# Performance work log

Hardware: AMD Instinct MI355X
Metric: run time of the kernel (lower is better)

## Reference

```python
import jax, jax.numpy as jnp
import numpy as np

N, FIN, FOUT = 4096, 512, 256
ALPHA = 0.2          # LeakyReLU negative slope
NEG_INF = -9e15      # mask value from the torch source


def setup_inputs() -> dict:
    key = jax.random.key(0)
    ks = jax.random.split(key, 11)
    h = jax.random.normal(ks[0], (N, FIN), dtype=jnp.float32)
    adj_n = jax.random.randint(ks[1], (N, N), 0, 2, dtype=jnp.int32)
    adj_d = jax.random.randint(ks[2], (N, N), 0, 2, dtype=jnp.int32)
    G_nd = jax.random.normal(ks[3], (2, N, FOUT), dtype=jnp.float32)
    # learned parameters (xavier-ish scale)
    W_n = jax.random.normal(ks[4], (FIN, FOUT), dtype=jnp.float32) * 0.05
    a1_n = jax.random.normal(ks[5], (FOUT, 1), dtype=jnp.float32) * 0.05
    a2_n = jax.random.normal(ks[6], (FOUT, 1), dtype=jnp.float32) * 0.05
    W_d = jax.random.normal(ks[7], (FIN, FOUT), dtype=jnp.float32) * 0.05
    a1_d = jax.random.normal(ks[8], (FOUT, 1), dtype=jnp.float32) * 0.05
    a2_d = jax.random.normal(ks[9], (FOUT, 1), dtype=jnp.float32) * 0.05
    scale = jnp.zeros((1,), dtype=jnp.float32)
    return {"h": h, "adj_n": adj_n, "adj_d": adj_d, "G_nd": G_nd,
            "W_n": W_n, "a1_n": a1_n, "a2_n": a2_n,
            "W_d": W_d, "a1_d": a1_d, "a2_d": a2_d, "scale": scale}


def _gat(h, adj, W, a1, a2):
    # Wh: [N, FOUT]
    Wh = h @ W
    # outer-sum attention logits: e[i,j] = leakyrelu(Wh_i.a1 + Wh_j.a2)
    e = jax.nn.leaky_relu((Wh @ a1) + (Wh @ a2).T, negative_slope=ALPHA)  # [N, N]
    att = jnp.where(adj > 0, e, jnp.float32(NEG_INF))
    att = jax.nn.softmax(att, axis=-1)
    # dropout is identity in eval mode
    return jax.nn.elu(att @ Wh)  # [N, FOUT]


def reference(h, adj_n, adj_d, G_nd, W_n, a1_n, a2_n, W_d, a1_d, a2_d, scale):
    f_n_S = _gat(h, adj_n, W_n, a1_n, a2_n)
    f_d_S = _gat(h, adj_d, W_d, a1_d, a2_d)
    # The G_nd cross-attention branch (f_nd_C) in the torch source is computed
    # but never used in the returned value; omitted here (jit would DCE it).
    return f_n_S + f_d_S
```

## Files before the change

### kernel.cpp

```cpp
#include <hip/hip_runtime.h>

#define N_NODES 4096
#define FIN     512
#define FOUT    256
#define NSPLIT  4
#define NTILES  ((N_NODES / NSPLIT) / 64)
#define ITILE   128

typedef __attribute__((ext_vector_type(8))) short bf16x8s;
typedef __attribute__((ext_vector_type(4))) float f32x4;
typedef __attribute__((ext_vector_type(8))) unsigned short u16x8;
typedef unsigned short u16;
typedef unsigned int   u32;

__device__ inline u16 f2b(float f) {
    union { float f; unsigned int u; } v; v.f = f;
    unsigned int r = v.u + 0x7fffu + ((v.u >> 16) & 1u);
    return (u16)(r >> 16);
}

__global__ __launch_bounds__(256) void prep_kernel(
    const float* __restrict__ h, const float* __restrict__ Wn,
    const float* __restrict__ Wd,
    u16* __restrict__ hb, u16* __restrict__ WTb, float* __restrict__ s12)
{
    __shared__ u16 tl[64 * 72];
    const int t = threadIdx.x;
    const int bid = blockIdx.x;

    if (bid < 1024) {
        int idx = (bid * 256 + t) * 8;
        float4 f0 = *(const float4*)&h[idx];
        float4 f1 = *(const float4*)&h[idx + 4];
        u16x8 o;
        o[0]=f2b(f0.x); o[1]=f2b(f0.y); o[2]=f2b(f0.z); o[3]=f2b(f0.w);
        o[4]=f2b(f1.x); o[5]=f2b(f1.y); o[6]=f2b(f1.z); o[7]=f2b(f1.w);
        *(u16x8*)&hb[idx] = o;
    } else if (bid < 1088) {
        int id = bid - 1024;
        int kx = id & 7, ny = (id >> 3) & 3, b = id >> 5;
        const float* W = b ? Wd : Wn;
        int k0 = kx * 64, n0 = ny * 64;
        int kr = t >> 2, nc0 = (t & 3) * 16;
        const float* src = W + (size_t)(k0 + kr) * FOUT + n0 + nc0;
        #pragma unroll
        for (int jv = 0; jv < 4; ++jv) {
            float4 f = *(const float4*)(src + jv * 4);
            tl[(nc0 + jv * 4 + 0) * 72 + kr] = f2b(f.x);
            tl[(nc0 + jv * 4 + 1) * 72 + kr] = f2b(f.y);
            tl[(nc0 + jv * 4 + 2) * 72 + kr] = f2b(f.z);
            tl[(nc0 + jv * 4 + 3) * 72 + kr] = f2b(f.w);
        }
        __syncthreads();
        int n = t >> 2, kc0 = (t & 3) * 16;
        u16* dst = WTb + ((size_t)b << 17) + (size_t)(n0 + n) * FIN + k0 + kc0;
        *(uint4*)dst       = *(uint4*)&tl[n * 72 + kc0];
        *(uint4*)(dst + 8) = *(uint4*)&tl[n * 72 + kc0 + 8];
    } else {
        float4 z = {0.f, 0.f, 0.f, 0.f};
        float4* p4 = (float4*)s12;
        #pragma unroll
        for (int k = 0; k < 16; ++k) p4[k * 256 + t] = z;
    }
}

__global__ __launch_bounds__(256) void wh_gemm_kernel(
    const u16* __restrict__ hb, const u16* __restrict__ WTb,
    const float* __restrict__ a1n, const float* __restrict__ a2n,
    const float* __restrict__ a1d, const float* __restrict__ a2d,
    u16* __restrict__ WhT, float* __restrict__ s1, float* __restrict__ s2)
{
    __shared__ u16 smem[8192];
    u16* a_lds = smem;
    u16* b_lds = smem + 4096;

    const int t = threadIdx.x, lane = t & 63, w = t >> 6;
    const int q = lane >> 4, ln = lane & 15;
    const int i0 = blockIdx.x * 64, n0 = blockIdx.y * 64, b = blockIdx.z;
    const u16* wt = WTb + ((size_t)b << 17);

    f32x4 acc[4];
    #pragma unroll
    for (int i = 0; i < 4; ++i) acc[i] = (f32x4){0.f, 0.f, 0.f, 0.f};

    for (int kt = 0; kt < 8; ++kt) {
        const int k0 = kt * 64;
        __syncthreads();
        #pragma unroll
        for (int it = 0; it < 2; ++it) {
            int chunk = it * 256 + t;
            int r = chunk >> 3, kc = chunk & 7;
            const u16* g = hb + (size_t)(i0 + r) * FIN + k0 + ((kc ^ (r & 7)) * 8);
            u16* l = a_lds + (it * 256 + w * 64) * 8;
            __builtin_amdgcn_global_load_lds(
                (const __attribute__((address_space(1))) void*)g,
                (__attribute__((address_space(3))) void*)l, 16, 0, 0);
        }
        #pragma unroll
        for (int it = 0; it < 2; ++it) {
            int chunk = it * 256 + t;
            int n = chunk >> 3, kc = chunk & 7;
            const u16* g = wt + (size_t)(n0 + n) * FIN + k0 + ((kc ^ (n & 7)) * 8);
            u16* l = b_lds + (it * 256 + w * 64) * 8;
            __builtin_amdgcn_global_load_lds(
                (const __attribute__((address_space(1))) void*)g,
                (__attribute__((address_space(3))) void*)l, 16, 0, 0);
        }
        __syncthreads();
        #pragma unroll
        for (int ks = 0; ks < 2; ++ks) {
            int sw = ((ks * 4 + q) ^ (ln & 7)) * 8;
            bf16x8s af = *(const bf16x8s*)&a_lds[(w * 16 + ln) * 64 + sw];
            #pragma unroll
            for (int nt = 0; nt < 4; ++nt) {
                bf16x8s bfv = *(const bf16x8s*)&b_lds[(nt * 16 + ln) * 64 + sw];
                acc[nt] = __builtin_amdgcn_mfma_f32_16x16x32_bf16(af, bfv, acc[nt], 0, 0, 0);
            }
        }
    }

    {
        const float* a1 = b ? a1d : a1n;
        const float* a2 = b ? a2d : a2n;
        float s1p[4] = {0.f, 0.f, 0.f, 0.f};
        float s2p[4] = {0.f, 0.f, 0.f, 0.f};
        #pragma unroll
        for (int nt = 0; nt < 4; ++nt) {
            float va1 = a1[n0 + nt * 16 + ln];
            float va2 = a2[n0 + nt * 16 + ln];
            #pragma unroll
            for (int r = 0; r < 4; ++r) {
                s1p[r] += acc[nt][r] * va1;
                s2p[r] += acc[nt][r] * va2;
            }
        }
        #pragma unroll
        for (int r = 0; r < 4; ++r) {
            #pragma unroll
            for (int off = 8; off >= 1; off >>= 1) {
                s1p[r] += __shfl_xor(s1p[r], off);
                s2p[r] += __shfl_xor(s2p[r], off);
            }
            if (ln == 0) {
                int row = i0 + w * 16 + q * 4 + r;
                atomicAdd(&s1[b * N_NODES + row], s1p[r]);
                atomicAdd(&s2[b * N_NODES + row], s2p[r]);
            }
        }
    }

    __syncthreads();
    #pragma unroll
    for (int nt = 0; nt < 4; ++nt)
        #pragma unroll
        for (int r = 0; r < 4; ++r)
            smem[(nt * 16 + ln) * 72 + (w * 16 + q * 4 + r)] = f2b(acc[nt][r]);
    __syncthreads();
    {
        const int nl = t >> 2, is = (t & 3) * 16;
        u16* dst = WhT + ((size_t)b << 20) + (size_t)(n0 + nl) * N_NODES + i0 + is;
        *(uint4*)dst       = *(uint4*)&smem[nl * 72 + is];
        *(uint4*)(dst + 8) = *(uint4*)&smem[nl * 72 + is + 8];
    }
}

__global__ __launch_bounds__(1024) void attn_kernel(
    const int* __restrict__ adj_n, const int* __restrict__ adj_d,
    const u16* __restrict__ WhT,
    const float* __restrict__ s1, const float* __restrict__ s2,
    float* __restrict__ num_ws, float* __restrict__ den_ws)
{
    __shared__ u16 wht_lds[256 * 64];
    __shared__ u16 p_lds[128 * 64];

    const int t = threadIdx.x, lane = t & 63, w = t >> 6;
    const int q = lane >> 4, ln = lane & 15;
    const int ih = w >> 2;
    const int nq = w & 3;
    const int b = blockIdx.z, split = blockIdx.y;
    const int i0 = blockIdx.x * ITILE;

    const int* adjb = b ? adj_d : adj_n;
    const u16* whtB = WhT + ((size_t)b << 20);
    const float* s1b = s1 + b * N_NODES;
    const float* s2b = s2 + b * N_NODES;

    const int pr = t >> 3;
    const int cw = t & 7;
    const int pc = cw * 8;
    const float s1v = s1b[i0 + pr];
    const size_t arow = (size_t)(i0 + pr) * N_NODES + pc;
    const int swp = (cw ^ (pr & 7)) * 8;

    float den0 = 0.f;

    f32x4 acc[2][4];
    #pragma unroll
    for (int mt = 0; mt < 2; ++mt)
        #pragma unroll
        for (int nt = 0; nt < 4; ++nt) acc[mt][nt] = (f32x4){0.f, 0.f, 0.f, 0.f};

    const int jbase = split * (N_NODES / NSPLIT);

    int4 a0_pf = *(const int4*)&adjb[arow + jbase];
    int4 a1_pf = *(const int4*)&adjb[arow + jbase + 4];
    float4 sv0_pf = *(const float4*)&s2b[jbase + pc];
    float4 sv1_pf = *(const float4*)&s2b[jbase + pc + 4];

    for (int jt = 0; jt < NTILES; ++jt) {
        const int j0 = jbase + jt * 64;
        __syncthreads();
        #pragma unroll
        for (int it = 0; it < 2; ++it) {
            int chunk = it * 1024 + t;
            int n = chunk >> 3, kc = chunk & 7;
            const u16* g = whtB + (size_t)n * N_NODES + j0 + ((kc ^ (n & 7)) * 8);
            u16* l = wht_lds + (it * 1024 + w * 64) * 8;
            __builtin_amdgcn_global_load_lds(
                (const __attribute__((address_space(1))) void*)g,
                (__attribute__((address_space(3))) void*)l, 16, 0, 0);
        }
        int4 a0 = a0_pf, a1 = a1_pf;
        float4 sv0 = sv0_pf, sv1 = sv1_pf;
        if (jt < NTILES - 1) {
            const int jn = j0 + 64;
            a0_pf = *(const int4*)&adjb[arow + jn];
            a1_pf = *(const int4*)&adjb[arow + jn + 4];
            sv0_pf = *(const float4*)&s2b[jn + pc];
            sv1_pf = *(const float4*)&s2b[jn + pc + 4];
        }
        int v[8] = {a0.x, a0.y, a0.z, a0.w, a1.x, a1.y, a1.z, a1.w};
        float svf[8] = {sv0.x, sv0.y, sv0.z, sv0.w, sv1.x, sv1.y, sv1.z, sv1.w};
        float d = 0.f;
        u16x8 pk;
        #pragma unroll
        for (int jj = 0; jj < 8; ++jj) {
            float x = s1v + svf[jj];
            float p = (v[jj] > 0) ? __expf(fmaxf(x, 0.2f * x)) : 0.f;
            d += p;
            pk[jj] = f2b(p);
        }
        d += __shfl_down(d, 4, 8);
        d += __shfl_down(d, 2, 8);
        d += __shfl_down(d, 1, 8);
        if ((t & 7) == 0) den0 += d;
        *(u16x8*)&p_lds[pr * 64 + swp] = pk;
        __syncthreads();
        #pragma unroll
        for (int ks = 0; ks < 2; ++ks) {
            int sw = ((ks * 4 + q) ^ (ln & 7)) * 8;
            bf16x8s af0 = *(const bf16x8s*)&p_lds[(ih * 32 + 0 * 16 + ln) * 64 + sw];
            bf16x8s af1 = *(const bf16x8s*)&p_lds[(ih * 32 + 1 * 16 + ln) * 64 + sw];
            #pragma unroll
            for (int nt = 0; nt < 4; ++nt) {
                bf16x8s bfv = *(const bf16x8s*)&wht_lds[(nq * 64 + nt * 16 + ln) * 64 + sw];
                acc[0][nt] = __builtin_amdgcn_mfma_f32_16x16x32_bf16(af0, bfv, acc[0][nt], 0, 0, 0);
                acc[1][nt] = __builtin_amdgcn_mfma_f32_16x16x32_bf16(af1, bfv, acc[1][nt], 0, 0, 0);
            }
        }
    }
    const size_t pbase = (size_t)(b * NSPLIT + split) * N_NODES;
    #pragma unroll
    for (int mt = 0; mt < 2; ++mt)
        #pragma unroll
        for (int r = 0; r < 4; ++r) {
            int row = ih * 32 + mt * 16 + q * 4 + r;
            #pragma unroll
            for (int nt = 0; nt < 4; ++nt)
                num_ws[(pbase + i0 + row) * FOUT + nq * 64 + nt * 16 + ln] = acc[mt][nt][r];
        }
    if ((t & 7) == 0) den_ws[pbase + i0 + pr] = den0;
}

__global__ __launch_bounds__(256) void reduce_kernel(
    const float* __restrict__ num_ws, const float* __restrict__ den_ws,
    float* __restrict__ out)
{
    int gid = blockIdx.x * 256 + threadIdx.x;
    int i = gid >> 6;
    int f4 = (gid & 63) * 4;
    float4 o = {0.f, 0.f, 0.f, 0.f};
    #pragma unroll
    for (int b = 0; b < 2; ++b) {
        float4 num = {0.f, 0.f, 0.f, 0.f};
        float den = 0.f;
        #pragma unroll
        for (int s = 0; s < NSPLIT; ++s) {
            const float4 v = *(const float4*)&num_ws[((size_t)(b * NSPLIT + s) * N_NODES + i) * FOUT + f4];
            num.x += v.x; num.y += v.y; num.z += v.z; num.w += v.w;
            den += den_ws[(size_t)(b * NSPLIT + s) * N_NODES + i];
        }
        float inv = 1.0f / den;
        float e0 = num.x * inv, e1 = num.y * inv, e2 = num.z * inv, e3 = num.w * inv;
        o.x += (e0 > 0.f) ? e0 : expm1f(e0);
        o.y += (e1 > 0.f) ? e1 : expm1f(e1);
        o.z += (e2 > 0.f) ? e2 : expm1f(e2);
        o.w += (e3 > 0.f) ? e3 : expm1f(e3);
    }
    *(float4*)&out[(size_t)i * FOUT + f4] = o;
}

extern "C" void kernel_launch(void* const* d_in, const int* in_sizes, int n_in,
                              void* d_out, int out_size, void* d_ws, size_t ws_size,
                              hipStream_t stream) {
    const float* h    = (const float*)d_in[0];
    const int*   adjn = (const int*)d_in[1];
    const int*   adjd = (const int*)d_in[2];
    const float* Wn   = (const float*)d_in[4];
    const float* a1n  = (const float*)d_in[5];
    const float* a2n  = (const float*)d_in[6];
    const float* Wd   = (const float*)d_in[7];
    const float* a1d  = (const float*)d_in[8];
    const float* a2d  = (const float*)d_in[9];

    char* ws = (char*)d_ws;
    u16*  WhT  = (u16*)ws;
    float* s1  = (float*)(ws + ((size_t)8 << 20));
    float* s2  = s1 + 2 * N_NODES;
    float* den = s2 + 2 * N_NODES;
    u16*  hb   = (u16*)(ws + ((size_t)8 << 20) + ((size_t)256 << 10));
    u16*  WTb  = (u16*)(ws + ((size_t)12 << 20) + ((size_t)256 << 10));
    float* num = (float*)(ws + ((size_t)8 << 20) + ((size_t)256 << 10));

    prep_kernel<<<1089, 256, 0, stream>>>(h, Wn, Wd, hb, WTb, s1);
    wh_gemm_kernel<<<dim3(64, 4, 2), 256, 0, stream>>>(hb, WTb, a1n, a2n, a1d, a2d, WhT, s1, s2);
    attn_kernel<<<dim3(N_NODES / ITILE, NSPLIT, 2), 1024, 0, stream>>>(adjn, adjd, WhT, s1, s2, num, den);
    reduce_kernel<<<1024, 256, 0, stream>>>(num, den, (float*)d_out);
}
```

Before: 215.9 us.

## Load MFMA B operands directly from global memory and double-buffer P tile

Both the Wh GEMM and the attention kernel stop staging operand tiles in LDS through global_load_lds and instead read each wave's MFMA fragments straight from global memory. The attention kernel keeps P in LDS but double-buffers it, which removes one barrier per tile. This cuts LDS traffic and synchronisation. In exchange, each WhT fragment is now re-read from global/L2 by the waves sharing it (every ih wave group) instead of being shared through LDS, and uncoalesced 16-byte row-strided loads with exposed latency may hurt.

After: 247.1 us. 14.5% more time.

```diff
diff --git a/kernel.cpp b/kernel.cpp
--- a/kernel.cpp
+++ b/kernel.cpp
@@ -70,52 +70,37 @@
     const float* __restrict__ a1d, const float* __restrict__ a2d,
     u16* __restrict__ WhT, float* __restrict__ s1, float* __restrict__ s2)
 {
-    __shared__ u16 smem[8192];
-    u16* a_lds = smem;
-    u16* b_lds = smem + 4096;
+    __shared__ u16 smem[64 * 72];
 
     const int t = threadIdx.x, lane = t & 63, w = t >> 6;
     const int q = lane >> 4, ln = lane & 15;
     const int i0 = blockIdx.x * 64, n0 = blockIdx.y * 64, b = blockIdx.z;
     const u16* wt = WTb + ((size_t)b << 17);
 
+    const u16* arow = hb + (size_t)(i0 + w * 16 + ln) * FIN;
+    const u16* brow0 = wt + (size_t)(n0 + 0 * 16 + ln) * FIN;
+    const u16* brow1 = wt + (size_t)(n0 + 1 * 16 + ln) * FIN;
+    const u16* brow2 = wt + (size_t)(n0 + 2 * 16 + ln) * FIN;
+    const u16* brow3 = wt + (size_t)(n0 + 3 * 16 + ln) * FIN;
+
     f32x4 acc[4];
     #pragma unroll
     for (int i = 0; i < 4; ++i) acc[i] = (f32x4){0.f, 0.f, 0.f, 0.f};
 
+    #pragma unroll
     for (int kt = 0; kt < 8; ++kt) {
-        const int k0 = kt * 64;
-        __syncthreads();
-        #pragma unroll
-        for (int it = 0; it < 2; ++it) {
-            int chunk = it * 256 + t;
-            int r = chunk >> 3, kc = chunk & 7;
-            const u16* g = hb + (size_t)(i0 + r) * FIN + k0 + ((kc ^ (r & 7)) * 8);
-            u16* l = a_lds + (it * 256 + w * 64) * 8;
-            __builtin_amdgcn_global_load_lds(
-                (const __attribute__((address_space(1))) void*)g,
-                (__attribute__((address_space(3))) void*)l, 16, 0, 0);
-        }
-        #pragma unroll
-        for (int it = 0; it < 2; ++it) {
-            int chunk = it * 256 + t;
-            int n = chunk >> 3, kc = chunk & 7;
-            const u16* g = wt + (size_t)(n0 + n) * FIN + k0 + ((kc ^ (n & 7)) * 8);
-            u16* l = b_lds + (it * 256 + w * 64) * 8;
-            __builtin_amdgcn_global_load_lds(
-                (const __attribute__((address_space(1))) void*)g,
-                (__attribute__((address_space(3))) void*)l, 16, 0, 0);
-        }
-        __syncthreads();
         #pragma unroll
         for (int ks = 0; ks < 2; ++ks) {
-            int sw = ((ks * 4 + q) ^ (ln & 7)) * 8;
-            bf16x8s af = *(const bf16x8s*)&a_lds[(w * 16 + ln) * 64 + sw];
-            #pragma unroll
-            for (int nt = 0; nt < 4; ++nt) {
-                bf16x8s bfv = *(const bf16x8s*)&b_lds[(nt * 16 + ln) * 64 + sw];
-                acc[nt] = __builtin_amdgcn_mfma_f32_16x16x32_bf16(af, bfv, acc[nt], 0, 0, 0);
-            }
+            const int ko = kt * 64 + (ks * 4 + q) * 8;
+            bf16x8s af = *(const bf16x8s*)&arow[ko];
+            bf16x8s b0 = *(const bf16x8s*)&brow0[ko];
+            bf16x8s b1 = *(const bf16x8s*)&brow1[ko];
+            bf16x8s b2 = *(const bf16x8s*)&brow2[ko];
+            bf16x8s b3 = *(const bf16x8s*)&brow3[ko];
+            acc[0] = __builtin_amdgcn_mfma_f32_16x16x32_bf16(af, b0, acc[0], 0, 0, 0);
+            acc[1] = __builtin_amdgcn_mfma_f32_16x16x32_bf16(af, b1, acc[1], 0, 0, 0);
+            acc[2] = __builtin_amdgcn_mfma_f32_16x16x32_bf16(af, b2, acc[2], 0, 0, 0);
+            acc[3] = __builtin_amdgcn_mfma_f32_16x16x32_bf16(af, b3, acc[3], 0, 0, 0);
         }
     }
 
@@ -170,8 +155,7 @@
     const float* __restrict__ s1, const float* __restrict__ s2,
     float* __restrict__ num_ws, float* __restrict__ den_ws)
 {
-    __shared__ u16 wht_lds[256 * 64];
-    __shared__ u16 p_lds[128 * 64];
+    __shared__ u16 p_lds[2][128 * 64];
 
     const int t = threadIdx.x, lane = t & 63, w = t >> 6;
     const int q = lane >> 4, ln = lane & 15;
@@ -185,6 +169,11 @@
     const float* s1b = s1 + b * N_NODES;
     const float* s2b = s2 + b * N_NODES;
 
+    const u16* brow0 = whtB + (size_t)(nq * 64 + 0 * 16 + ln) * N_NODES;
+    const u16* brow1 = whtB + (size_t)(nq * 64 + 1 * 16 + ln) * N_NODES;
+    const u16* brow2 = whtB + (size_t)(nq * 64 + 2 * 16 + ln) * N_NODES;
+    const u16* brow3 = whtB + (size_t)(nq * 64 + 3 * 16 + ln) * N_NODES;
+
     const int pr = t >> 3;
     const int cw = t & 7;
     const int pc = cw * 8;
@@ -209,17 +198,8 @@
 
     for (int jt = 0; jt < NTILES; ++jt) {
         const int j0 = jbase + jt * 64;
-        __syncthreads();
-        #pragma unroll
-        for (int it = 0; it < 2; ++it) {
-            int chunk = it * 1024 + t;
-            int n = chunk >> 3, kc = chunk & 7;
-            const u16* g = whtB + (size_t)n * N_NODES + j0 + ((kc ^ (n & 7)) * 8);
-            u16* l = wht_lds + (it * 1024 + w * 64) * 8;
-            __builtin_amdgcn_global_load_lds(
-                (const __attribute__((address_space(1))) void*)g,
-                (__attribute__((address_space(3))) void*)l, 16, 0, 0);
-        }
+        const int cur = jt & 1;
+
         int4 a0 = a0_pf, a1 = a1_pf;
         float4 sv0 = sv0_pf, sv1 = sv1_pf;
         if (jt < NTILES - 1) {
@@ -244,19 +224,26 @@
         d += __shfl_down(d, 2, 8);
         d += __shfl_down(d, 1, 8);
         if ((t & 7) == 0) den0 += d;
-        *(u16x8*)&p_lds[pr * 64 + swp] = pk;
+        *(u16x8*)&p_lds[cur][pr * 64 + swp] = pk;
         __syncthreads();
         #pragma unroll
         for (int ks = 0; ks < 2; ++ks) {
-            int sw = ((ks * 4 + q) ^ (ln & 7)) * 8;
-            bf16x8s af0 = *(const bf16x8s*)&p_lds[(ih * 32 + 0 * 16 + ln) * 64 + sw];
-            bf16x8s af1 = *(const bf16x8s*)&p_lds[(ih * 32 + 1 * 16 + ln) * 64 + sw];
-            #pragma unroll
-            for (int nt = 0; nt < 4; ++nt) {
-                bf16x8s bfv = *(const bf16x8s*)&wht_lds[(nq * 64 + nt * 16 + ln) * 64 + sw];
-                acc[0][nt] = __builtin_amdgcn_mfma_f32_16x16x32_bf16(af0, bfv, acc[0][nt], 0, 0, 0);
-                acc[1][nt] = __builtin_amdgcn_mfma_f32_16x16x32_bf16(af1, bfv, acc[1][nt], 0, 0, 0);
-            }
+            const int sw = ((ks * 4 + q) ^ (ln & 7)) * 8;
+            const int ko = j0 + (ks * 4 + q) * 8;
+            bf16x8s af0 = *(const bf16x8s*)&p_lds[cur][(ih * 32 + 0 * 16 + ln) * 64 + sw];
+            bf16x8s af1 = *(const bf16x8s*)&p_lds[cur][(ih * 32 + 1 * 16 + ln) * 64 + sw];
+            bf16x8s b0 = *(const bf16x8s*)&brow0[ko];
+            bf16x8s b1 = *(const bf16x8s*)&brow1[ko];
+            bf16x8s b2 = *(const bf16x8s*)&brow2[ko];
+            bf16x8s b3 = *(const bf16x8s*)&brow3[ko];
+            acc[0][0] = __builtin_amdgcn_mfma_f32_16x16x32_bf16(af0, b0, acc[0][0], 0, 0, 0);
+            acc[1][0] = __builtin_amdgcn_mfma_f32_16x16x32_bf16(af1, b0, acc[1][0], 0, 0, 0);
+            acc[0][1] = __builtin_amdgcn_mfma_f32_16x16x32_bf16(af0, b1, acc[0][1], 0, 0, 0);
+            acc[1][1] = __builtin_amdgcn_mfma_f32_16x16x32_bf16(af1, b1, acc[1][1], 0, 0, 0);
+            acc[0][2] = __builtin_amdgcn_mfma_f32_16x16x32_bf16(af0, b2, acc[0][2], 0, 0, 0);
+            acc[1][2] = __builtin_amdgcn_mfma_f32_16x16x32_bf16(af1, b2, acc[1][2], 0, 0, 0);
+            acc[0][3] = __builtin_amdgcn_mfma_f32_16x16x32_bf16(af0, b3, acc[0][3], 0, 0, 0);
+            acc[1][3] = __builtin_amdgcn_mfma_f32_16x16x32_bf16(af1, b3, acc[1][3], 0, 0, 0);
         }
     }
     const size_t pbase = (size_t)(b * NSPLIT + split) * N_NODES;
```

## Fuse prep, GEMM, attention and reduce into one cooperative kernel

Applied to the files above, without the earlier changes.

Merges the four launches (bf16 conversion/transpose, Wh GEMM with score projections, masked-softmax attention GEMM, split reduction with ELU) into one cooperative kernel of 256 blocks × 1024 threads, with grid.sync between phases. The goal is to remove per-launch overhead and the idle gaps between dependent kernels. In exchange it adds three grid-wide barriers, and the GEMM phase runs on only half the blocks, with four 256-thread groups sharing a block. It also switches the in-loop bf16 pack to the library conversion intrinsic.

After: 330.0 us. 52.9% more time.

```diff
diff --git a/kernel.cpp b/kernel.cpp
--- a/kernel.cpp
+++ b/kernel.cpp
@@ -1,4 +1,8 @@
 #include <hip/hip_runtime.h>
+#include <hip/hip_bf16.h>
+#include <hip/hip_cooperative_groups.h>
+
+namespace cg = cooperative_groups;
 
 #define N_NODES 4096
 #define FIN     512
@@ -11,7 +15,6 @@
 typedef __attribute__((ext_vector_type(4))) float f32x4;
 typedef __attribute__((ext_vector_type(8))) unsigned short u16x8;
 typedef unsigned short u16;
-typedef unsigned int   u32;
 
 __device__ inline u16 f2b(float f) {
     union { float f; unsigned int u; } v; v.f = f;
@@ -19,29 +22,42 @@
     return (u16)(r >> 16);
 }
 
-__global__ __launch_bounds__(256) void prep_kernel(
-    const float* __restrict__ h, const float* __restrict__ Wn,
-    const float* __restrict__ Wd,
-    u16* __restrict__ hb, u16* __restrict__ WTb, float* __restrict__ s12)
+__device__ inline u16 f2b_fast(float f) {
+    return __bfloat16_as_ushort(__float2bfloat16(f));
+}
+
+__global__ __launch_bounds__(1024) void fused_kernel(
+    const float* __restrict__ h,
+    const int* __restrict__ adj_n, const int* __restrict__ adj_d,
+    const float* __restrict__ Wn, const float* __restrict__ a1n, const float* __restrict__ a2n,
+    const float* __restrict__ Wd, const float* __restrict__ a1d, const float* __restrict__ a2d,
+    u16* __restrict__ hb, u16* __restrict__ WTb, u16* __restrict__ WhT,
+    float* __restrict__ s1, float* __restrict__ s2,
+    float* __restrict__ num_ws, float* __restrict__ den_ws,
+    float* __restrict__ out)
 {
-    __shared__ u16 tl[64 * 72];
+    __shared__ __align__(16) u16 smem[32768];
+    cg::grid_group grid = cg::this_grid();
+    const int B = blockIdx.x;
     const int t = threadIdx.x;
-    const int bid = blockIdx.x;
-
-    if (bid < 1024) {
-        int idx = (bid * 256 + t) * 8;
+
+    {
+        int idx = (B * 1024 + t) * 8;
         float4 f0 = *(const float4*)&h[idx];
         float4 f1 = *(const float4*)&h[idx + 4];
         u16x8 o;
         o[0]=f2b(f0.x); o[1]=f2b(f0.y); o[2]=f2b(f0.z); o[3]=f2b(f0.w);
         o[4]=f2b(f1.x); o[5]=f2b(f1.y); o[6]=f2b(f1.z); o[7]=f2b(f1.w);
         *(u16x8*)&hb[idx] = o;
-    } else if (bid < 1088) {
-        int id = bid - 1024;
-        int kx = id & 7, ny = (id >> 3) & 3, b = id >> 5;
-        const float* W = b ? Wd : Wn;
-        int k0 = kx * 64, n0 = ny * 64;
-        int kr = t >> 2, nc0 = (t & 3) * 16;
+    }
+    if (B < 16) {
+        const int g = t >> 8, tg = t & 255;
+        const int id = B * 4 + g;
+        const int kx = id & 7, ny = (id >> 3) & 3, bb = id >> 5;
+        const float* W = bb ? Wd : Wn;
+        const int k0 = kx * 64, n0 = ny * 64;
+        u16* tl = smem + g * 4608;
+        int kr = tg >> 2, nc0 = (tg & 3) * 16;
         const float* src = W + (size_t)(k0 + kr) * FOUT + n0 + nc0;
         #pragma unroll
         for (int jv = 0; jv < 4; ++jv) {
@@ -52,252 +68,242 @@
             tl[(nc0 + jv * 4 + 3) * 72 + kr] = f2b(f.w);
         }
         __syncthreads();
-        int n = t >> 2, kc0 = (t & 3) * 16;
-        u16* dst = WTb + ((size_t)b << 17) + (size_t)(n0 + n) * FIN + k0 + kc0;
+        int n = tg >> 2, kc0 = (tg & 3) * 16;
+        u16* dst = WTb + ((size_t)bb << 17) + (size_t)(n0 + n) * FIN + k0 + kc0;
         *(uint4*)dst       = *(uint4*)&tl[n * 72 + kc0];
         *(uint4*)(dst + 8) = *(uint4*)&tl[n * 72 + kc0 + 8];
-    } else {
+    } else if (B == 16) {
         float4 z = {0.f, 0.f, 0.f, 0.f};
-        float4* p4 = (float4*)s12;
-        #pragma unroll
-        for (int k = 0; k < 16; ++k) p4[k * 256 + t] = z;
-    }
-}
-
-__global__ __launch_bounds__(256) void wh_gemm_kernel(
-    const u16* __restrict__ hb, const u16* __restrict__ WTb,
-    const float* __restrict__ a1n, const float* __restrict__ a2n,
-    const float* __restrict__ a1d, const float* __restrict__ a2d,
-    u16* __restrict__ WhT, float* __restrict__ s1, float* __restrict__ s2)
-{
-    __shared__ u16 smem[8192];
-    u16* a_lds = smem;
-    u16* b_lds = smem + 4096;
-
-    const int t = threadIdx.x, lane = t & 63, w = t >> 6;
-    const int q = lane >> 4, ln = lane & 15;
-    const int i0 = blockIdx.x * 64, n0 = blockIdx.y * 64, b = blockIdx.z;
-    const u16* wt = WTb + ((size_t)b << 17);
-
-    f32x4 acc[4];
-    #pragma unroll
-    for (int i = 0; i < 4; ++i) acc[i] = (f32x4){0.f, 0.f, 0.f, 0.f};
-
-    for (int kt = 0; kt < 8; ++kt) {
-        const int k0 = kt * 64;
+        float4* p4 = (float4*)s1;
+        #pragma unroll
+        for (int k = 0; k < 4; ++k) p4[k * 1024 + t] = z;
+    }
+    grid.sync();
+
+    if (B < 128) {
+        const int g = t >> 8, tg = t & 255;
+        u16* gbase = smem + g * 8192;
+        u16* a_lds = gbase;
+        u16* b_lds = gbase + 4096;
+        const int sub = B * 4 + g;
+        const int i0 = (sub & 63) * 64, n0 = ((sub >> 6) & 3) * 64, bb = sub >> 8;
+        const int lane = tg & 63, w = tg >> 6;
+        const int q = lane >> 4, ln = lane & 15;
+        const u16* wt = WTb + ((size_t)bb << 17);
+
+        f32x4 acc[4];
+        #pragma unroll
+        for (int i = 0; i < 4; ++i) acc[i] = (f32x4){0.f, 0.f, 0.f, 0.f};
+
+        for (int kt = 0; kt < 8; ++kt) {
+            const int k0 = kt * 64;
+            __syncthreads();
+            #pragma unroll
+            for (int it = 0; it < 2; ++it) {
+                int chunk = it * 256 + tg;
+                int r = chunk >> 3, kc = chunk & 7;
+                const u16* gp = hb + (size_t)(i0 + r) * FIN + k0 + ((kc ^ (r & 7)) * 8);
+                u16* l = a_lds + (it * 256 + w * 64) * 8;
+                __builtin_amdgcn_global_load_lds(
+                    (const __attribute__((address_space(1))) void*)gp,
+                    (__attribute__((address_space(3))) void*)l, 16, 0, 0);
+            }
+            #pragma unroll
+            for (int it = 0; it < 2; ++it) {
+                int chunk = it * 256 + tg;
+                int n = chunk >> 3, kc = chunk & 7;
+                const u16* gp = wt + (size_t)(n0 + n) * FIN + k0 + ((kc ^ (n & 7)) * 8);
+                u16* l = b_lds + (it * 256 + w * 64) * 8;
+                __builtin_amdgcn_global_load_lds(
+                    (const __attribute__((address_space(1))) void*)gp,
+                    (__attribute__((address_space(3))) void*)l, 16, 0, 0);
+            }
+            __syncthreads();
+            #pragma unroll
+            for (int ks = 0; ks < 2; ++ks) {
+                int sw = ((ks * 4 + q) ^ (ln & 7)) * 8;
+                bf16x8s af = *(const bf16x8s*)&a_lds[(w * 16 + ln) * 64 + sw];
+                #pragma unroll
+                for (int nt = 0; nt < 4; ++nt) {
+                    bf16x8s bfv = *(const bf16x8s*)&b_lds[(nt * 16 + ln) * 64 + sw];
+                    acc[nt] = __builtin_amdgcn_mfma_f32_16x16x32_bf16(af, bfv, acc[nt], 0, 0, 0);
+                }
+            }
+        }
+        {
+            const float* a1 = bb ? a1d : a1n;
+            const float* a2 = bb ? a2d : a2n;
+            float s1p[4] = {0.f, 0.f, 0.f, 0.f};
+            float s2p[4] = {0.f, 0.f, 0.f, 0.f};
+            #pragma unroll
+            for (int nt = 0; nt < 4; ++nt) {
+                float va1 = a1[n0 + nt * 16 + ln];
+                float va2 = a2[n0 + nt * 16 + ln];
+                #pragma unroll
+                for (int r = 0; r < 4; ++r) {
+                    s1p[r] += acc[nt][r] * va1;
+                    s2p[r] += acc[nt][r] * va2;
+                }
+            }
+            #pragma unroll
+            for (int r = 0; r < 4; ++r) {
+                #pragma unroll
+                for (int off = 8; off >= 1; off >>= 1) {
+                    s1p[r] += __shfl_xor(s1p[r], off);
+                    s2p[r] += __shfl_xor(s2p[r], off);
+                }
+                if (ln == 0) {
+                    int row = i0 + w * 16 + q * 4 + r;
+                    atomicAdd(&s1[bb * N_NODES + row], s1p[r]);
+                    atomicAdd(&s2[bb * N_NODES + row], s2p[r]);
+                }
+            }
+        }
         __syncthreads();
         #pragma unroll
-        for (int it = 0; it < 2; ++it) {
-            int chunk = it * 256 + t;
-            int r = chunk >> 3, kc = chunk & 7;
-            const u16* g = hb + (size_t)(i0 + r) * FIN + k0 + ((kc ^ (r & 7)) * 8);
-            u16* l = a_lds + (it * 256 + w * 64) * 8;
-            __builtin_amdgcn_global_load_lds(
-                (const __attribute__((address_space(1))) void*)g,
-                (__attribute__((address_space(3))) void*)l, 16, 0, 0);
-        }
-        #pragma unroll
-        for (int it = 0; it < 2; ++it) {
-            int chunk = it * 256 + t;
-            int n = chunk >> 3, kc = chunk & 7;
-            const u16* g = wt + (size_t)(n0 + n) * FIN + k0 + ((kc ^ (n & 7)) * 8);
-            u16* l = b_lds + (it * 256 + w * 64) * 8;
-            __builtin_amdgcn_global_load_lds(
-                (const __attribute__((address_space(1))) void*)g,
-                (__attribute__((address_space(3))) void*)l, 16, 0, 0);
-        }
+        for (int nt = 0; nt < 4; ++nt)
+            #pragma unroll
+            for (int r = 0; r < 4; ++r)
+                gbase[(nt * 16 + ln) * 72 + (w * 16 + q * 4 + r)] = f2b(acc[nt][r]);
         __syncthreads();
-        #pragma unroll
-        for (int ks = 0; ks < 2; ++ks) {
-            int sw = ((ks * 4 + q) ^ (ln & 7)) * 8;
-            bf16x8s af = *(const bf16x8s*)&a_lds[(w * 16 + ln) * 64 + sw];
-            #pragma unroll
-            for (int nt = 0; nt < 4; ++nt) {
-                bf16x8s bfv = *(const bf16x8s*)&b_lds[(nt * 16 + ln) * 64 + sw];
-                acc[nt] = __builtin_amdgcn_mfma_f32_16x16x32_bf16(af, bfv, acc[nt], 0, 0, 0);
-            }
-        }
-    }
+        {
+            const int nl = tg >> 2, is = (tg & 3) * 16;
+            u16* dst = WhT + ((size_t)bb << 20) + (size_t)(n0 + nl) * N_NODES + i0 + is;
+            *(uint4*)dst       = *(uint4*)&gbase[nl * 72 + is];
+            *(uint4*)(dst + 8) = *(uint4*)&gbase[nl * 72 + is + 8];
+        }
+    }
+    grid.sync();
 
     {
-        const float* a1 = b ? a1d : a1n;
-        const float* a2 = b ? a2d : a2n;
-        float s1p[4] = {0.f, 0.f, 0.f, 0.f};
-        float s2p[4] = {0.f, 0.f, 0.f, 0.f};
-        #pragma unroll
-        for (int nt = 0; nt < 4; ++nt) {
-            float va1 = a1[n0 + nt * 16 + ln];
-            float va2 = a2[n0 + nt * 16 + ln];
+        u16* wht_lds = smem;
+        u16* p_lds   = smem + 16384;
+
+        const int lane = t & 63, w = t >> 6;
+        const int q = lane >> 4, ln = lane & 15;
+        const int ih = w >> 2;
+        const int nq = w & 3;
+        const int bb = B >> 7;
+        const int split = (B >> 5) & 3;
+        const int i0 = (B & 31) * ITILE;
+
+        const int* adjb = bb ? adj_d : adj_n;
+        const u16* whtB = WhT + ((size_t)bb << 20);
+        const float* s1b = s1 + bb * N_NODES;
+        const float* s2b = s2 + bb * N_NODES;
+
+        const int pr = t >> 3;
+        const int cw = t & 7;
+        const int pc = cw * 8;
+        const float s1v = s1b[i0 + pr];
+        const size_t arow = (size_t)(i0 + pr) * N_NODES + pc;
+        const int swp = (cw ^ (pr & 7)) * 8;
+
+        float den0 = 0.f;
+
+        f32x4 acc[2][4];
+        #pragma unroll
+        for (int mt = 0; mt < 2; ++mt)
+            #pragma unroll
+            for (int nt = 0; nt < 4; ++nt) acc[mt][nt] = (f32x4){0.f, 0.f, 0.f, 0.f};
+
+        const int jbase = split * (N_NODES / NSPLIT);
+
+        int4 a0_pf = *(const int4*)&adjb[arow + jbase];
+        int4 a1_pf = *(const int4*)&adjb[arow + jbase + 4];
+        float4 sv0_pf = *(const float4*)&s2b[jbase + pc];
+        float4 sv1_pf = *(const float4*)&s2b[jbase + pc + 4];
+
+        for (int jt = 0; jt < NTILES; ++jt) {
+            const int j0 = jbase + jt * 64;
+            __syncthreads();
+            #pragma unroll
+            for (int it = 0; it < 2; ++it) {
+                int chunk = it * 1024 + t;
+                int n = chunk >> 3, kc = chunk & 7;
+                const u16* gp = whtB + (size_t)n * N_NODES + j0 + ((kc ^ (n & 7)) * 8);
+                u16* l = wht_lds + (it * 1024 + w * 64) * 8;
+                __builtin_amdgcn_global_load_lds(
+                    (const __attribute__((address_space(1))) void*)gp,
+                    (__attribute__((address_space(3))) void*)l, 16, 0, 0);
+            }
+            int4 a0 = a0_pf, a1 = a1_pf;
+            float4 sv0 = sv0_pf, sv1 = sv1_pf;
+            if (jt < NTILES - 1) {
+                const int jn = j0 + 64;
+                a0_pf = *(const int4*)&adjb[arow + jn];
+                a1_pf = *(const int4*)&adjb[arow + jn + 4];
+                sv0_pf = *(const float4*)&s2b[jn + pc];
+                sv1_pf = *(const float4*)&s2b[jn + pc + 4];
+            }
+            int v[8] = {a0.x, a0.y, a0.z, a0.w, a1.x, a1.y, a1.z, a1.w};
+            float svf[8] = {sv0.x, sv0.y, sv0.z, sv0.w, sv1.x, sv1.y, sv1.z, sv1.w};
+            float d = 0.f;
+            u16x8 pk;
+            #pragma unroll
+            for (int jj = 0; jj < 8; ++jj) {
+                float x = s1v + svf[jj];
+                float p = (v[jj] > 0) ? __expf(fmaxf(x, 0.2f * x)) : 0.f;
+                d += p;
+                pk[jj] = f2b_fast(p);
+            }
+            d += __shfl_down(d, 4, 8);
+            d += __shfl_down(d, 2, 8);
+            d += __shfl_down(d, 1, 8);
+            if ((t & 7) == 0) den0 += d;
+            *(u16x8*)&p_lds[pr * 64 + swp] = pk;
+            __syncthreads();
+            #pragma unroll
+            for (int ks = 0; ks < 2; ++ks) {
+                int sw = ((ks * 4 + q) ^ (ln & 7)) * 8;
+                bf16x8s af0 = *(const bf16x8s*)&p_lds[(ih * 32 + 0 * 16 + ln) * 64 + sw];
+                bf16x8s af1 = *(const bf16x8s*)&p_lds[(ih * 32 + 1 * 16 + ln) * 64 + sw];
+                #pragma unroll
+                for (int nt = 0; nt < 4; ++nt) {
+                    bf16x8s bfv = *(const bf16x8s*)&wht_lds[(nq * 64 + nt * 16 + ln) * 64 + sw];
+                    acc[0][nt] = __builtin_amdgcn_mfma_f32_16x16x32_bf16(af0, bfv, acc[0][nt], 0, 0, 0);
+                    acc[1][nt] = __builtin_amdgcn_mfma_f32_16x16x32_bf16(af1, bfv, acc[1][nt], 0, 0, 0);
+                }
+            }
+        }
+        const size_t pbase = (size_t)(bb * NSPLIT + split) * N_NODES;
+        #pragma unroll
+        for (int mt = 0; mt < 2; ++mt)
             #pragma unroll
             for (int r = 0; r < 4; ++r) {
-                s1p[r] += acc[nt][r] * va1;
-                s2p[r] += acc[nt][r] * va2;
-            }
-        }
-        #pragma unroll
-        for (int r = 0; r < 4; ++r) {
-            #pragma unroll
-            for (int off = 8; off >= 1; off >>= 1) {
-                s1p[r] += __shfl_xor(s1p[r], off);
-                s2p[r] += __shfl_xor(s2p[r], off);
-            }
-            if (ln == 0) {
-                int row = i0 + w * 16 + q * 4 + r;
-                atomicAdd(&s1[b * N_NODES + row], s1p[r]);
-                atomicAdd(&s2[b * N_NODES + row], s2p[r]);
-            }
-        }
-    }
-
-    __syncthreads();
-    #pragma unroll
-    for (int nt = 0; nt < 4; ++nt)
-        #pragma unroll
-        for (int r = 0; r < 4; ++r)
-            smem[(nt * 16 + ln) * 72 + (w * 16 + q * 4 + r)] = f2b(acc[nt][r]);
-    __syncthreads();
+                int row = ih * 32 + mt * 16 + q * 4 + r;
+                #pragma unroll
+                for (int nt = 0; nt < 4; ++nt)
+                    num_ws[(pbase + i0 + row) * FOUT + nq * 64 + nt * 16 + ln] = acc[mt][nt][r];
+            }
+        if ((t & 7) == 0) den_ws[pbase + i0 + pr] = den0;
+    }
+    grid.sync();
+
     {
-        const int nl = t >> 2, is = (t & 3) * 16;
-        u16* dst = WhT + ((size_t)b << 20) + (size_t)(n0 + nl) * N_NODES + i0 + is;
-        *(uint4*)dst       = *(uint4*)&smem[nl * 72 + is];
-        *(uint4*)(dst + 8) = *(uint4*)&smem[nl * 72 + is + 8];
-    }
-}
-
-__global__ __launch_bounds__(1024) void attn_kernel(
-    const int* __restrict__ adj_n, const int* __restrict__ adj_d,
-    const u16* __restrict__ WhT,
-    const float* __restrict__ s1, const float* __restrict__ s2,
-    float* __restrict__ num_ws, float* __restrict__ den_ws)
-{
-    __shared__ u16 wht_lds[256 * 64];
-    __shared__ u16 p_lds[128 * 64];
-
-    const int t = threadIdx.x, lane = t & 63, w = t >> 6;
-    const int q = lane >> 4, ln = lane & 15;
-    const int ih = w >> 2;
-    const int nq = w & 3;
-    const int b = blockIdx.z, split = blockIdx.y;
-    const int i0 = blockIdx.x * ITILE;
-
-    const int* adjb = b ? adj_d : adj_n;
-    const u16* whtB = WhT + ((size_t)b << 20);
-    const float* s1b = s1 + b * N_NODES;
-    const float* s2b = s2 + b * N_NODES;
-
-    const int pr = t >> 3;
-    const int cw = t & 7;
-    const int pc = cw * 8;
-    const float s1v = s1b[i0 + pr];
-    const size_t arow = (size_t)(i0 + pr) * N_NODES + pc;
-    const int swp = (cw ^ (pr & 7)) * 8;
-
-    float den0 = 0.f;
-
-    f32x4 acc[2][4];
-    #pragma unroll
-    for (int mt = 0; mt < 2; ++mt)
-        #pragma unroll
-        for (int nt = 0; nt < 4; ++nt) acc[mt][nt] = (f32x4){0.f, 0.f, 0.f, 0.f};
-
-    const int jbase = split * (N_NODES / NSPLIT);
-
-    int4 a0_pf = *(const int4*)&adjb[arow + jbase];
-    int4 a1_pf = *(const int4*)&adjb[arow + jbase + 4];
-    float4 sv0_pf = *(const float4*)&s2b[jbase + pc];
-    float4 sv1_pf = *(const float4*)&s2b[jbase + pc + 4];
-
-    for (int jt = 0; jt < NTILES; ++jt) {
-        const int j0 = jbase + jt * 64;
-        __syncthreads();
-        #pragma unroll
-        for (int it = 0; it < 2; ++it) {
-            int chunk = it * 1024 + t;
-            int n = chunk >> 3, kc = chunk & 7;
-            const u16* g = whtB + (size_t)n * N_NODES + j0 + ((kc ^ (n & 7)) * 8);
-            u16* l = wht_lds + (it * 1024 + w * 64) * 8;
-            __builtin_amdgcn_global_load_lds(
-                (const __attribute__((address_space(1))) void*)g,
-                (__attribute__((address_space(3))) void*)l, 16, 0, 0);
-        }
-        int4 a0 = a0_pf, a1 = a1_pf;
-        float4 sv0 = sv0_pf, sv1 = sv1_pf;
-        if (jt < NTILES - 1) {
-            const int jn = j0 + 64;
-            a0_pf = *(const int4*)&adjb[arow + jn];
-            a1_pf = *(const int4*)&adjb[arow + jn + 4];
-            sv0_pf = *(const float4*)&s2b[jn + pc];
-            sv1_pf = *(const float4*)&s2b[jn + pc + 4];
-        }
-        int v[8] = {a0.x, a0.y, a0.z, a0.w, a1.x, a1.y, a1.z, a1.w};
-        float svf[8] = {sv0.x, sv0.y, sv0.z, sv0.w, sv1.x, sv1.y, sv1.z, sv1.w};
-        float d = 0.f;
-        u16x8 pk;
-        #pragma unroll
-        for (int jj = 0; jj < 8; ++jj) {
-            float x = s1v + svf[jj];
-            float p = (v[jj] > 0) ? __expf(fmaxf(x, 0.2f * x)) : 0.f;
-            d += p;
-            pk[jj] = f2b(p);
-        }
-        d += __shfl_down(d, 4, 8);
-        d += __shfl_down(d, 2, 8);
-        d += __shfl_down(d, 1, 8);
-        if ((t & 7) == 0) den0 += d;
-        *(u16x8*)&p_lds[pr * 64 + swp] = pk;
-        __syncthreads();
-        #pragma unroll
-        for (int ks = 0; ks < 2; ++ks) {
-            int sw = ((ks * 4 + q) ^ (ln & 7)) * 8;
-            bf16x8s af0 = *(const bf16x8s*)&p_lds[(ih * 32 + 0 * 16 + ln) * 64 + sw];
-            bf16x8s af1 = *(const bf16x8s*)&p_lds[(ih * 32 + 1 * 16 + ln) * 64 + sw];
-            #pragma unroll
-            for (int nt = 0; nt < 4; ++nt) {
-                bf16x8s bfv = *(const bf16x8s*)&wht_lds[(nq * 64 + nt * 16 + ln) * 64 + sw];
-                acc[0][nt] = __builtin_amdgcn_mfma_f32_16x16x32_bf16(af0, bfv, acc[0][nt], 0, 0, 0);
-                acc[1][nt] = __builtin_amdgcn_mfma_f32_16x16x32_bf16(af1, bfv, acc[1][nt], 0, 0, 0);
-            }
-        }
-    }
-    const size_t pbase = (size_t)(b * NSPLIT + split) * N_NODES;
-    #pragma unroll
-    for (int mt = 0; mt < 2; ++mt)
-        #pragma unroll
-        for (int r = 0; r < 4; ++r) {
-            int row = ih * 32 + mt * 16 + q * 4 + r;
-            #pragma unroll
-            for (int nt = 0; nt < 4; ++nt)
-                num_ws[(pbase + i0 + row) * FOUT + nq * 64 + nt * 16 + ln] = acc[mt][nt][r];
-        }
-    if ((t & 7) == 0) den_ws[pbase + i0 + pr] = den0;
-}
-
-__global__ __launch_bounds__(256) void reduce_kernel(
-    const float* __restrict__ num_ws, const float* __restrict__ den_ws,
-    float* __restrict__ out)
-{
-    int gid = blockIdx.x * 256 + threadIdx.x;
-    int i = gid >> 6;
-    int f4 = (gid & 63) * 4;
-    float4 o = {0.f, 0.f, 0.f, 0.f};
-    #pragma unroll
-    for (int b = 0; b < 2; ++b) {
-        float4 num = {0.f, 0.f, 0.f, 0.f};
-        float den = 0.f;
-        #pragma unroll
-        for (int s = 0; s < NSPLIT; ++s) {
-            const float4 v = *(const float4*)&num_ws[((size_t)(b * NSPLIT + s) * N_NODES + i) * FOUT + f4];
-            num.x += v.x; num.y += v.y; num.z += v.z; num.w += v.w;
-            den += den_ws[(size_t)(b * NSPLIT + s) * N_NODES + i];
-        }
-        float inv = 1.0f / den;
-        float e0 = num.x * inv, e1 = num.y * inv, e2 = num.z * inv, e3 = num.w * inv;
-        o.x += (e0 > 0.f) ? e0 : expm1f(e0);
-        o.y += (e1 > 0.f) ? e1 : expm1f(e1);
-        o.z += (e2 > 0.f) ? e2 : expm1f(e2);
-        o.w += (e3 > 0.f) ? e3 : expm1f(e3);
-    }
-    *(float4*)&out[(size_t)i * FOUT + f4] = o;
+        int gid = B * 1024 + t;
+        int i = gid >> 6;
+        int f4 = (gid & 63) * 4;
+        float4 o = {0.f, 0.f, 0.f, 0.f};
+        #pragma unroll
+        for (int bb = 0; bb < 2; ++bb) {
+            float4 numv = {0.f, 0.f, 0.f, 0.f};
+            float den = 0.f;
+            #pragma unroll
+            for (int s = 0; s < NSPLIT; ++s) {
+                const float4 v = *(const float4*)&num_ws[((size_t)(bb * NSPLIT + s) * N_NODES + i) * FOUT + f4];
+                numv.x += v.x; numv.y += v.y; numv.z += v.z; numv.w += v.w;
+                den += den_ws[(size_t)(bb * NSPLIT + s) * N_NODES + i];
+            }
+            float inv = 1.0f / den;
+            float e0 = numv.x * inv, e1 = numv.y * inv, e2 = numv.z * inv, e3 = numv.w * inv;
+            o.x += (e0 > 0.f) ? e0 : expm1f(e0);
+            o.y += (e1 > 0.f) ? e1 : expm1f(e1);
+            o.z += (e2 > 0.f) ? e2 : expm1f(e2);
+            o.w += (e3 > 0.f) ? e3 : expm1f(e3);
+        }
+        *(float4*)&out[(size_t)i * FOUT + f4] = o;
+    }
 }
 
 extern "C" void kernel_launch(void* const* d_in, const int* in_sizes, int n_in,
@@ -321,9 +327,17 @@
     u16*  hb   = (u16*)(ws + ((size_t)8 << 20) + ((size_t)256 << 10));
     u16*  WTb  = (u16*)(ws + ((size_t)12 << 20) + ((size_t)256 << 10));
     float* num = (float*)(ws + ((size_t)8 << 20) + ((size_t)256 << 10));
-
-    prep_kernel<<<1089, 256, 0, stream>>>(h, Wn, Wd, hb, WTb, s1);
-    wh_gemm_kernel<<<dim3(64, 4, 2), 256, 0, stream>>>(hb, WTb, a1n, a2n, a1d, a2d, WhT, s1, s2);
-    attn_kernel<<<dim3(N_NODES / ITILE, NSPLIT, 2), 1024, 0, stream>>>(adjn, adjd, WhT, s1, s2, num, den);
-    reduce_kernel<<<1024, 256, 0, stream>>>(num, den, (float*)d_out);
+    float* outp = (float*)d_out;
+
+    void* args[] = {
+        (void*)&h, (void*)&adjn, (void*)&adjd,
+        (void*)&Wn, (void*)&a1n, (void*)&a2n,
+        (void*)&Wd, (void*)&a1d, (void*)&a2d,
+        (void*)&hb, (void*)&WTb, (void*)&WhT,
+        (void*)&s1, (void*)&s2,
+        (void*)&num, (void*)&den,
+        (void*)&outp
+    };
+    hipLaunchCooperativeKernel((void*)fused_kernel, dim3(256), dim3(1024),
+                               args, 0, stream);
 }
```
